# Performance work log

Measured on AMD Instinct MI355X. Metric: run time of the kernel, lower is better.

Reference implementation:

```python
import jax, jax.numpy as jnp
import numpy as np

HEAD_SIZE = 64
N_EMBED = 768
B, T = 16, 2048


def setup_inputs() -> dict:
    key = jax.random.key(0)
    ks = jax.random.split(key, 7)
    return {
        "x": jax.random.normal(ks[0], (B, T, N_EMBED), dtype=jnp.float32),
        "v1": jax.random.normal(ks[1], (B, T, HEAD_SIZE), dtype=jnp.float32),
        "Wk": jax.random.normal(ks[2], (N_EMBED, HEAD_SIZE), dtype=jnp.float32) * 0.02,
        "Wq": jax.random.normal(ks[3], (N_EMBED, HEAD_SIZE), dtype=jnp.float32) * 0.02,
        "Wv": jax.random.normal(ks[4], (N_EMBED, HEAD_SIZE), dtype=jnp.float32) * 0.02,
        "Wproj": jax.random.normal(ks[5], (HEAD_SIZE, HEAD_SIZE), dtype=jnp.float32) * 0.02,
        "bproj": jnp.zeros((HEAD_SIZE,), dtype=jnp.float32),
        "lamb": jnp.float32(0.5),
    }


def reference(x, v1, Wk, Wq, Wv, Wproj, bproj, lamb):
    # x: [B, T, C]; single-head causal attention with value-residual mixing.
    k = x @ Wk  # [B, T, H]
    q = x @ Wq
    v = x @ Wv
    v = (1.0 - lamb) * v + lamb * v1  # value-residual mix
    scale = jnp.float32(1.0 / np.sqrt(HEAD_SIZE))
    w = jnp.einsum("bth,bsh->bts", q, k) * scale  # [B, T, T]
    t = x.shape[1]
    causal = jnp.tril(jnp.ones((t, t), dtype=bool))  # [T, T]
    w = jnp.where(causal, w, jnp.float32(-jnp.inf))
    w = jax.nn.softmax(w, axis=-1)
    # dropout is identity in eval mode
    out = jnp.einsum("bts,bsh->bth", w, v)  # [B, T, H]
    return out @ Wproj + bproj, v1
```

## Files before the change

kernel.cpp:

```cpp
#include <hip/hip_runtime.h>
#include <hip/hip_bf16.h>


constexpr int BATCH = 16;
constexpr int TSEQ  = 2048;
constexpr int CEMB  = 768;
constexpr int HS    = 64;
constexpr size_t NTOK    = (size_t)BATCH * TSEQ;
constexpr size_t OUTHALF = NTOK * HS;

typedef __bf16 bf16x4 __attribute__((ext_vector_type(4)));
typedef __bf16 bf16x8 __attribute__((ext_vector_type(8)));
typedef float  f32x4  __attribute__((ext_vector_type(4)));
typedef float  f32x16 __attribute__((ext_vector_type(16)));
typedef int    i32x4  __attribute__((ext_vector_type(4)));

__global__ __launch_bounds__(256) void prep_kernel(
    const float* __restrict__ wk, const float* __restrict__ wq,
    const float* __restrict__ wv, const float* __restrict__ wproj,
    __bf16* __restrict__ wt, __bf16* __restrict__ wpt)
{
    __shared__ __bf16 t[64][66];
    const int bid = blockIdx.x;
    if (bid < 36) {
        const int m = bid / 12, c0 = (bid % 12) * 64;
        const float* src = (m == 0) ? wk : (m == 1) ? wq : wv;
        for (int i = threadIdx.x; i < 4096; i += 256) {
            const int c = i >> 6, h = i & 63;
            t[c][h] = (__bf16)src[(size_t)(c0 + c) * HS + h];
        }
        __syncthreads();
        for (int i = threadIdx.x; i < 4096; i += 256) {
            const int h = i >> 6, c = i & 63;
            wt[(size_t)m * HS * CEMB + (size_t)h * CEMB + c0 + c] = t[c][h];
        }
    } else {
        for (int i = threadIdx.x; i < 4096; i += 256) {
            const int h = i >> 6, hp = i & 63;
            t[h][hp] = (__bf16)wproj[i];
        }
        __syncthreads();
        for (int i = threadIdx.x; i < 4096; i += 256) {
            const int hp = i >> 6, h = i & 63;
            wpt[i] = t[h][hp];
        }
    }
}

__global__ __launch_bounds__(256, 2) void qkv_kernel(
    const float* __restrict__ x,
    const float* __restrict__ v1,
    const __bf16* __restrict__ wt,
    const float* __restrict__ lamb_p,
    __bf16* __restrict__ kk,
    __bf16* __restrict__ qq,
    __bf16* __restrict__ vt,
    float* __restrict__ v1out)
{
    __shared__ __bf16 xl[2][64][88];

    const int wave = threadIdx.x >> 6;
    const int lane = threadIdx.x & 63;
    const int l16  = lane & 15;
    const int quad = lane >> 4;
    const size_t row0 = (size_t)blockIdx.x * 64;

    const int tok_s = threadIdx.x >> 2;
    const int cq    = threadIdx.x & 3;
    const float* xsrc = x + (row0 + tok_s) * CEMB + cq * 16;

    const __bf16* wbase[3];
    #pragma unroll
    for (int m = 0; m < 3; ++m)
        wbase[m] = wt + ((size_t)m * HS + wave * 16 + l16) * CEMB + quad * 8;

    f32x4 acc[3][4];
    #pragma unroll
    for (int m = 0; m < 3; ++m)
        #pragma unroll
        for (int rt = 0; rt < 4; ++rt)
            acc[m][rt] = (f32x4){0.f, 0.f, 0.f, 0.f};

    {
        f32x4 t0 = *(const f32x4*)(xsrc);
        f32x4 t1 = *(const f32x4*)(xsrc + 4);
        f32x4 t2 = *(const f32x4*)(xsrc + 8);
        f32x4 t3 = *(const f32x4*)(xsrc + 12);
        bf16x8 lo, hi;
        #pragma unroll
        for (int i = 0; i < 4; ++i) {
            lo[i] = (__bf16)t0[i]; lo[i + 4] = (__bf16)t1[i];
            hi[i] = (__bf16)t2[i]; hi[i + 4] = (__bf16)t3[i];
        }
        *(bf16x8*)&xl[0][tok_s][cq * 16]     = lo;
        *(bf16x8*)&xl[0][tok_s][cq * 16 + 8] = hi;
    }
    bf16x8 wc[3][2];
    #pragma unroll
    for (int m = 0; m < 3; ++m)
        #pragma unroll
        for (int ks = 0; ks < 2; ++ks)
            wc[m][ks] = *(const bf16x8*)(wbase[m] + ks * 32);
    __syncthreads();

    for (int c0 = 0; c0 < CEMB; c0 += 64) {
        const int buf = (c0 >> 6) & 1;
        const bool notlast = (c0 + 64 < CEMB);

        f32x4 nx0, nx1, nx2, nx3;
        bf16x8 wn[3][2];
        if (notlast) {
            const float* xs = xsrc + c0 + 64;
            nx0 = *(const f32x4*)(xs);
            nx1 = *(const f32x4*)(xs + 4);
            nx2 = *(const f32x4*)(xs + 8);
            nx3 = *(const f32x4*)(xs + 12);
            #pragma unroll
            for (int m = 0; m < 3; ++m)
                #pragma unroll
                for (int ks = 0; ks < 2; ++ks)
                    wn[m][ks] = *(const bf16x8*)(wbase[m] + c0 + 64 + ks * 32);
        }

        #pragma unroll
        for (int ks = 0; ks < 2; ++ks) {
            bf16x8 a[4];
            #pragma unroll
            for (int rt = 0; rt < 4; ++rt)
                a[rt] = *(const bf16x8*)&xl[buf][rt * 16 + l16][ks * 32 + quad * 8];
            #pragma unroll
            for (int m = 0; m < 3; ++m)
                #pragma unroll
                for (int rt = 0; rt < 4; ++rt)
                    acc[m][rt] = __builtin_amdgcn_mfma_f32_16x16x32_bf16(
                        a[rt], wc[m][ks], acc[m][rt], 0, 0, 0);
        }

        if (notlast) {
            bf16x8 lo, hi;
            #pragma unroll
            for (int i = 0; i < 4; ++i) {
                lo[i] = (__bf16)nx0[i]; lo[i + 4] = (__bf16)nx1[i];
                hi[i] = (__bf16)nx2[i]; hi[i + 4] = (__bf16)nx3[i];
            }
            *(bf16x8*)&xl[buf ^ 1][tok_s][cq * 16]     = lo;
            *(bf16x8*)&xl[buf ^ 1][tok_s][cq * 16 + 8] = hi;
            #pragma unroll
            for (int m = 0; m < 3; ++m)
                #pragma unroll
                for (int ks = 0; ks < 2; ++ks)
                    wc[m][ks] = wn[m][ks];
            __syncthreads();
        }
    }

    const float lam = lamb_p[0];
    const int col = wave * 16 + l16;
    const int b  = (int)(row0 >> 11);
    __bf16* vtb = vt + (size_t)b * HS * TSEQ + (size_t)col * TSEQ;
    #pragma unroll
    for (int rt = 0; rt < 4; ++rt) {
        const size_t tok0 = row0 + rt * 16 + quad * 4;
        bf16x4 pk;
        #pragma unroll
        for (int r = 0; r < 4; ++r) {
            const size_t idx = (tok0 + r) * HS + col;
            const float v1v = v1[idx];
            kk[idx] = (__bf16)acc[0][rt][r];
            qq[idx] = (__bf16)acc[1][rt][r];
            pk[r] = (__bf16)((1.0f - lam) * acc[2][rt][r] + lam * v1v);
            if (v1out) v1out[idx] = v1v;
        }
        *(bf16x4*)(vtb + (tok0 & 2047)) = pk;
    }
}

__device__ __forceinline__ int pk2(float lo, float hi) {
    unsigned short a = __builtin_bit_cast(unsigned short, (__bf16)lo);
    unsigned short b = __builtin_bit_cast(unsigned short, (__bf16)hi);
    return (int)((((unsigned)b) << 16) | (unsigned)a);
}
__device__ __forceinline__ bf16x8 make_bfrag(const float* p, int hi) {
    const int a0 = pk2(p[0], p[1]), a1 = pk2(p[2], p[3]);
    const int b0 = pk2(p[4], p[5]), b1 = pk2(p[6], p[7]);
    const int pa0 = __shfl_xor(a0, 32), pa1 = __shfl_xor(a1, 32);
    const int pb0 = __shfl_xor(b0, 32), pb1 = __shfl_xor(b1, 32);
    i32x4 w;
    w[0] = hi ? pb0 : a0;
    w[1] = hi ? pb1 : a1;
    w[2] = hi ? b0  : pa0;
    w[3] = hi ? b1  : pa1;
    return __builtin_bit_cast(bf16x8, w);
}

__global__ __launch_bounds__(256, 2) void attn_kernel(
    const __bf16* __restrict__ q,
    const __bf16* __restrict__ k,
    const __bf16* __restrict__ vt,
    const __bf16* __restrict__ wpt,
    const float* __restrict__ bproj,
    float* __restrict__ y)
{
    __shared__ float olds[4][64][32];
    __shared__ float mred[4][32];
    __shared__ float lred[4][32];

    const int b    = blockIdx.x >> 5;
    const int jp   = blockIdx.x & 31;
    const int wave = threadIdx.x >> 6;
    const int lane = threadIdx.x & 63;
    const int l31  = lane & 31;
    const int hi   = lane >> 5;
    const int hi8  = hi * 8;

    const __bf16* kb = k  + (size_t)b * TSEQ * HS;
    const __bf16* vb = vt + (size_t)b * HS * TSEQ;
    const float sc2 = 0.125f * 1.44269504f;

    bf16x8 wf[4];
    if (wave < 2) {
        const __bf16* wp = wpt + (size_t)(wave * 32 + l31) * HS + hi8;
        #pragma unroll
        for (int c = 0; c < 4; ++c) wf[c] = *(const bf16x8*)(wp + c * 16);
    }

    for (int pass = 0; pass < 2; ++pass) {
        const int j = pass ? (63 - jp) : jp;
        const size_t tok0 = (size_t)b * TSEQ + (size_t)j * 32;

        const __bf16* qp = q + (tok0 + l31) * HS + hi8;
        bf16x8 qf[4];
        #pragma unroll
        for (int c = 0; c < 4; ++c) qf[c] = *(const bf16x8*)(qp + c * 16);

        f32x16 o0, o1;
        #pragma unroll
        for (int r = 0; r < 16; ++r) { o0[r] = 0.f; o1[r] = 0.f; }
        float m_i = -1e30f, l_i = 0.f;

        bf16x8 kf[4], kn[4], vf[4], vn[4];
        if (wave <= j) {
            const int s0 = wave * 32;
            const __bf16* kp = kb + (size_t)(s0 + l31) * HS + hi8;
            #pragma unroll
            for (int c = 0; c < 4; ++c) kf[c] = *(const bf16x8*)(kp + c * 16);
            #pragma unroll
            for (int ht = 0; ht < 2; ++ht)
                #pragma unroll
                for (int c2 = 0; c2 < 2; ++c2)
                    vf[ht * 2 + c2] = *(const bf16x8*)(vb
                        + (size_t)(ht * 32 + l31) * TSEQ + s0 + c2 * 16 + hi8);
        }

        for (int t = wave; t <= j; t += 4) {
            const int s0 = t * 32;
            const bool more = (t + 4 <= j);
            if (more) {
                const int sn = s0 + 128;
                const __bf16* kp = kb + (size_t)(sn + l31) * HS + hi8;
                #pragma unroll
                for (int c = 0; c < 4; ++c) kn[c] = *(const bf16x8*)(kp + c * 16);
                #pragma unroll
                for (int ht = 0; ht < 2; ++ht)
                    #pragma unroll
                    for (int c2 = 0; c2 < 2; ++c2)
                        vn[ht * 2 + c2] = *(const bf16x8*)(vb
                            + (size_t)(ht * 32 + l31) * TSEQ + sn + c2 * 16 + hi8);
            }

            f32x16 s;
            #pragma unroll
            for (int r = 0; r < 16; ++r) s[r] = 0.f;
            __builtin_amdgcn_s_setprio(1);
            #pragma unroll
            for (int c = 0; c < 4; ++c)
                s = __builtin_amdgcn_mfma_f32_32x32x16_bf16(kf[c], qf[c], s, 0, 0, 0);
            __builtin_amdgcn_s_setprio(0);

            float p[16];
            if (t == j) {
                #pragma unroll
                for (int r = 0; r < 16; ++r) {
                    const int krow = (r & 3) + 8 * (r >> 2) + 4 * hi;
                    p[r] = (krow <= l31) ? s[r] * sc2 : -1e30f;
                }
            } else {
                #pragma unroll
                for (int r = 0; r < 16; ++r) p[r] = s[r] * sc2;
            }

            float x0 = fmaxf(p[0], p[1]),   x1 = fmaxf(p[2], p[3]);
            float x2 = fmaxf(p[4], p[5]),   x3 = fmaxf(p[6], p[7]);
            float x4 = fmaxf(p[8], p[9]),   x5 = fmaxf(p[10], p[11]);
            float x6 = fmaxf(p[12], p[13]), x7 = fmaxf(p[14], p[15]);
            float mx = fmaxf(fmaxf(fmaxf(x0, x1), fmaxf(x2, x3)),
                             fmaxf(fmaxf(x4, x5), fmaxf(x6, x7)));
            mx = fmaxf(mx, __shfl_xor(mx, 32));

            if (!__all(mx <= m_i + 8.f)) {
                const float mn = fmaxf(m_i, mx);
                const float alpha = exp2f(m_i - mn);
                m_i = mn;
                l_i *= alpha;
                #pragma unroll
                for (int r = 0; r < 16; ++r) { o0[r] *= alpha; o1[r] *= alpha; }
            }

            #pragma unroll
            for (int r = 0; r < 16; ++r) p[r] = exp2f(p[r] - m_i);

            float r0 = (p[0] + p[1]) + (p[2] + p[3]);
            float r1 = (p[4] + p[5]) + (p[6] + p[7]);
            float r2 = (p[8] + p[9]) + (p[10] + p[11]);
            float r3 = (p[12] + p[13]) + (p[14] + p[15]);
            float rs = (r0 + r1) + (r2 + r3);
            rs += __shfl_xor(rs, 32);
            l_i += rs;

            const bf16x8 fb0 = make_bfrag(&p[0], hi);
            const bf16x8 fb1 = make_bfrag(&p[8], hi);

            __builtin_amdgcn_s_setprio(1);
            o0 = __builtin_amdgcn_mfma_f32_32x32x16_bf16(vf[0], fb0, o0, 0, 0, 0);
            o0 = __builtin_amdgcn_mfma_f32_32x32x16_bf16(vf[1], fb1, o0, 0, 0, 0);
            o1 = __builtin_amdgcn_mfma_f32_32x32x16_bf16(vf[2], fb0, o1, 0, 0, 0);
            o1 = __builtin_amdgcn_mfma_f32_32x32x16_bf16(vf[3], fb1, o1, 0, 0, 0);
            __builtin_amdgcn_s_setprio(0);

            if (more) {
                #pragma unroll
                for (int c = 0; c < 4; ++c) { kf[c] = kn[c]; vf[c] = vn[c]; }
            }
        }

        #pragma unroll
        for (int r = 0; r < 16; ++r) {
            const int row = (r & 3) + 8 * (r >> 2) + 4 * hi;
            olds[wave][row][l31]      = o0[r];
            olds[wave][row + 32][l31] = o1[r];
        }
        if (lane < 32) { mred[wave][lane] = m_i; lred[wave][lane] = l_i; }
        __syncthreads();

        if (wave < 2) {
            float mw[4], lw[4];
            #pragma unroll
            for (int w = 0; w < 4; ++w) { mw[w] = mred[w][l31]; lw[w] = lred[w][l31]; }
            const float mg = fmaxf(fmaxf(mw[0], mw[1]), fmaxf(mw[2], mw[3]));
            float g[4], lg = 0.f;
            #pragma unroll
            for (int w = 0; w < 4; ++w) { g[w] = exp2f(mw[w] - mg); lg += g[w] * lw[w]; }
            const float inv = 1.0f / lg;

            float on[32];
            #pragma unroll
            for (int r = 0; r < 16; ++r) {
                const int row = (r & 3) + 8 * (r >> 2) + 4 * hi;
                float a0 = 0.f, a1 = 0.f;
                #pragma unroll
                for (int w = 0; w < 4; ++w) {
                    a0 += g[w] * olds[w][row][l31];
                    a1 += g[w] * olds[w][row + 32][l31];
                }
                on[r]      = a0 * inv;
                on[r + 16] = a1 * inv;
            }

            f32x16 res;
            #pragma unroll
            for (int r = 0; r < 16; ++r) res[r] = 0.f;
            #pragma unroll
            for (int c = 0; c < 4; ++c) {
                const bf16x8 ob = make_bfrag(&on[c * 8], hi);
                res = __builtin_amdgcn_mfma_f32_32x32x16_bf16(wf[c], ob, res, 0, 0, 0);
            }

            float* yp = y + (tok0 + l31) * HS + wave * 32;
            #pragma unroll
            for (int grp = 0; grp < 4; ++grp) {
                const f32x4 bb = *(const f32x4*)(bproj + wave * 32 + grp * 8 + 4 * hi);
                f32x4 o4;
                #pragma unroll
                for (int rr = 0; rr < 4; ++rr) o4[rr] = res[grp * 4 + rr] + bb[rr];
                *(f32x4*)(yp + grp * 8 + 4 * hi) = o4;
            }
        }
        __syncthreads();
    }
}

__global__ __launch_bounds__(256) void copy_kernel(
    const float* __restrict__ src, float* __restrict__ dst)
{
    const size_t i = ((size_t)blockIdx.x * 256 + threadIdx.x) * 4;
    *(f32x4*)(dst + i) = *(const f32x4*)(src + i);
}

extern "C" void kernel_launch(void* const* d_in, const int* in_sizes, int n_in,
                              void* d_out, int out_size, void* d_ws, size_t ws_size,
                              hipStream_t stream) {
    const float* x     = (const float*)d_in[0];
    const float* v1    = (const float*)d_in[1];
    const float* wk    = (const float*)d_in[2];
    const float* wq    = (const float*)d_in[3];
    const float* wv    = (const float*)d_in[4];
    const float* wproj = (const float*)d_in[5];
    const float* bproj = (const float*)d_in[6];
    const float* lamb  = (const float*)d_in[7];

    float* out = (float*)d_out;

    __bf16* qp  = (__bf16*)d_ws;
    __bf16* wt  = qp + OUTHALF;
    __bf16* wpt = wt + (size_t)3 * HS * CEMB;
    const size_t base_elems = OUTHALF + (size_t)3 * HS * CEMB + (size_t)HS * HS;
    const size_t need_bytes = (base_elems + 2 * OUTHALF) * sizeof(__bf16);

    __bf16* kp;
    __bf16* vtp;
    float*  v1out;
    const bool fused_v1 = (ws_size >= need_bytes);
    if (fused_v1) {
        kp    = wpt + (size_t)HS * HS;
        vtp   = kp + OUTHALF;
        v1out = out + OUTHALF;
    } else {
        kp    = (__bf16*)(out + OUTHALF);
        vtp   = kp + OUTHALF;
        v1out = nullptr;
    }

    prep_kernel<<<dim3(37), dim3(256), 0, stream>>>(wk, wq, wv, wproj, wt, wpt);

    qkv_kernel<<<dim3((int)(NTOK / 64)), dim3(256), 0, stream>>>(
        x, v1, wt, lamb, kp, qp, vtp, v1out);

    attn_kernel<<<dim3(BATCH * 32), dim3(256), 0, stream>>>(
        qp, kp, vtp, wpt, bproj, out);

    if (!fused_v1) {
        copy_kernel<<<dim3((int)(OUTHALF / (256 * 4))), dim3(256), 0, stream>>>(
            v1, out + OUTHALF);
    }
}
```

Before: 237.5 us.

## Halve block work in QKV and attention kernels, raise occupancy to four blocks

```diff
diff --git a/kernel.cpp b/kernel.cpp
--- a/kernel.cpp
+++ b/kernel.cpp
@@ -47,7 +47,7 @@
     }
 }
 
-__global__ __launch_bounds__(256, 2) void qkv_kernel(
+__global__ __launch_bounds__(256, 4) void qkv_kernel(
     const float* __restrict__ x,
     const float* __restrict__ v1,
     const __bf16* __restrict__ wt,
@@ -57,43 +57,37 @@
     __bf16* __restrict__ vt,
     float* __restrict__ v1out)
 {
-    __shared__ __bf16 xl[2][64][88];
+    __shared__ __bf16 xl[2][32][88];
 
     const int wave = threadIdx.x >> 6;
     const int lane = threadIdx.x & 63;
     const int l16  = lane & 15;
     const int quad = lane >> 4;
-    const size_t row0 = (size_t)blockIdx.x * 64;
-
-    const int tok_s = threadIdx.x >> 2;
-    const int cq    = threadIdx.x & 3;
-    const float* xsrc = x + (row0 + tok_s) * CEMB + cq * 16;
+    const size_t row0 = (size_t)blockIdx.x * 32;
+
+    const int tok_s = threadIdx.x >> 3;
+    const int cq    = threadIdx.x & 7;
+    const float* xsrc = x + (row0 + tok_s) * CEMB + cq * 8;
 
     const __bf16* wbase[3];
     #pragma unroll
     for (int m = 0; m < 3; ++m)
         wbase[m] = wt + ((size_t)m * HS + wave * 16 + l16) * CEMB + quad * 8;
 
-    f32x4 acc[3][4];
+    f32x4 acc[3][2];
     #pragma unroll
     for (int m = 0; m < 3; ++m)
         #pragma unroll
-        for (int rt = 0; rt < 4; ++rt)
+        for (int rt = 0; rt < 2; ++rt)
             acc[m][rt] = (f32x4){0.f, 0.f, 0.f, 0.f};
 
     {
         f32x4 t0 = *(const f32x4*)(xsrc);
         f32x4 t1 = *(const f32x4*)(xsrc + 4);
-        f32x4 t2 = *(const f32x4*)(xsrc + 8);
-        f32x4 t3 = *(const f32x4*)(xsrc + 12);
-        bf16x8 lo, hi;
-        #pragma unroll
-        for (int i = 0; i < 4; ++i) {
-            lo[i] = (__bf16)t0[i]; lo[i + 4] = (__bf16)t1[i];
-            hi[i] = (__bf16)t2[i]; hi[i + 4] = (__bf16)t3[i];
-        }
-        *(bf16x8*)&xl[0][tok_s][cq * 16]     = lo;
-        *(bf16x8*)&xl[0][tok_s][cq * 16 + 8] = hi;
+        bf16x8 v;
+        #pragma unroll
+        for (int i = 0; i < 4; ++i) { v[i] = (__bf16)t0[i]; v[i + 4] = (__bf16)t1[i]; }
+        *(bf16x8*)&xl[0][tok_s][cq * 8] = v;
     }
     bf16x8 wc[3][2];
     #pragma unroll
@@ -107,14 +101,12 @@
         const int buf = (c0 >> 6) & 1;
         const bool notlast = (c0 + 64 < CEMB);
 
-        f32x4 nx0, nx1, nx2, nx3;
+        f32x4 nx0, nx1;
         bf16x8 wn[3][2];
         if (notlast) {
             const float* xs = xsrc + c0 + 64;
             nx0 = *(const f32x4*)(xs);
             nx1 = *(const f32x4*)(xs + 4);
-            nx2 = *(const f32x4*)(xs + 8);
-            nx3 = *(const f32x4*)(xs + 12);
             #pragma unroll
             for (int m = 0; m < 3; ++m)
                 #pragma unroll
@@ -124,27 +116,23 @@
 
         #pragma unroll
         for (int ks = 0; ks < 2; ++ks) {
-            bf16x8 a[4];
-            #pragma unroll
-            for (int rt = 0; rt < 4; ++rt)
+            bf16x8 a[2];
+            #pragma unroll
+            for (int rt = 0; rt < 2; ++rt)
                 a[rt] = *(const bf16x8*)&xl[buf][rt * 16 + l16][ks * 32 + quad * 8];
             #pragma unroll
             for (int m = 0; m < 3; ++m)
                 #pragma unroll
-                for (int rt = 0; rt < 4; ++rt)
+                for (int rt = 0; rt < 2; ++rt)
                     acc[m][rt] = __builtin_amdgcn_mfma_f32_16x16x32_bf16(
                         a[rt], wc[m][ks], acc[m][rt], 0, 0, 0);
         }
 
         if (notlast) {
-            bf16x8 lo, hi;
-            #pragma unroll
-            for (int i = 0; i < 4; ++i) {
-                lo[i] = (__bf16)nx0[i]; lo[i + 4] = (__bf16)nx1[i];
-                hi[i] = (__bf16)nx2[i]; hi[i + 4] = (__bf16)nx3[i];
-            }
-            *(bf16x8*)&xl[buf ^ 1][tok_s][cq * 16]     = lo;
-            *(bf16x8*)&xl[buf ^ 1][tok_s][cq * 16 + 8] = hi;
+            bf16x8 v;
+            #pragma unroll
+            for (int i = 0; i < 4; ++i) { v[i] = (__bf16)nx0[i]; v[i + 4] = (__bf16)nx1[i]; }
+            *(bf16x8*)&xl[buf ^ 1][tok_s][cq * 8] = v;
             #pragma unroll
             for (int m = 0; m < 3; ++m)
                 #pragma unroll
@@ -159,7 +147,7 @@
     const int b  = (int)(row0 >> 11);
     __bf16* vtb = vt + (size_t)b * HS * TSEQ + (size_t)col * TSEQ;
     #pragma unroll
-    for (int rt = 0; rt < 4; ++rt) {
+    for (int rt = 0; rt < 2; ++rt) {
         const size_t tok0 = row0 + rt * 16 + quad * 4;
         bf16x4 pk;
         #pragma unroll
@@ -193,7 +181,7 @@
     return __builtin_bit_cast(bf16x8, w);
 }
 
-__global__ __launch_bounds__(256, 2) void attn_kernel(
+__global__ __launch_bounds__(256, 4) void attn_kernel(
     const __bf16* __restrict__ q,
     const __bf16* __restrict__ k,
     const __bf16* __restrict__ vt,
@@ -205,8 +193,8 @@
     __shared__ float mred[4][32];
     __shared__ float lred[4][32];
 
-    const int b    = blockIdx.x >> 5;
-    const int jp   = blockIdx.x & 31;
+    const int b    = blockIdx.x >> 6;
+    const int j    = blockIdx.x & 63;
     const int wave = threadIdx.x >> 6;
     const int lane = threadIdx.x & 63;
     const int l31  = lane & 31;
@@ -224,168 +212,164 @@
         for (int c = 0; c < 4; ++c) wf[c] = *(const bf16x8*)(wp + c * 16);
     }
 
-    for (int pass = 0; pass < 2; ++pass) {
-        const int j = pass ? (63 - jp) : jp;
-        const size_t tok0 = (size_t)b * TSEQ + (size_t)j * 32;
-
-        const __bf16* qp = q + (tok0 + l31) * HS + hi8;
-        bf16x8 qf[4];
-        #pragma unroll
-        for (int c = 0; c < 4; ++c) qf[c] = *(const bf16x8*)(qp + c * 16);
-
-        f32x16 o0, o1;
-        #pragma unroll
-        for (int r = 0; r < 16; ++r) { o0[r] = 0.f; o1[r] = 0.f; }
-        float m_i = -1e30f, l_i = 0.f;
-
-        bf16x8 kf[4], kn[4], vf[4], vn[4];
-        if (wave <= j) {
-            const int s0 = wave * 32;
-            const __bf16* kp = kb + (size_t)(s0 + l31) * HS + hi8;
-            #pragma unroll
-            for (int c = 0; c < 4; ++c) kf[c] = *(const bf16x8*)(kp + c * 16);
+    const size_t tok0 = (size_t)b * TSEQ + (size_t)j * 32;
+
+    const __bf16* qp = q + (tok0 + l31) * HS + hi8;
+    bf16x8 qf[4];
+    #pragma unroll
+    for (int c = 0; c < 4; ++c) qf[c] = *(const bf16x8*)(qp + c * 16);
+
+    f32x16 o0, o1;
+    #pragma unroll
+    for (int r = 0; r < 16; ++r) { o0[r] = 0.f; o1[r] = 0.f; }
+    float m_i = -1e30f, l_i = 0.f;
+
+    bf16x8 kf[4], kn[4], vf[4], vn[4];
+    if (wave <= j) {
+        const int s0 = wave * 32;
+        const __bf16* kp = kb + (size_t)(s0 + l31) * HS + hi8;
+        #pragma unroll
+        for (int c = 0; c < 4; ++c) kf[c] = *(const bf16x8*)(kp + c * 16);
+        #pragma unroll
+        for (int ht = 0; ht < 2; ++ht)
+            #pragma unroll
+            for (int c2 = 0; c2 < 2; ++c2)
+                vf[ht * 2 + c2] = *(const bf16x8*)(vb
+                    + (size_t)(ht * 32 + l31) * TSEQ + s0 + c2 * 16 + hi8);
+    }
+
+    for (int t = wave; t <= j; t += 4) {
+        const int s0 = t * 32;
+        const bool more = (t + 4 <= j);
+        if (more) {
+            const int sn = s0 + 128;
+            const __bf16* kp = kb + (size_t)(sn + l31) * HS + hi8;
+            #pragma unroll
+            for (int c = 0; c < 4; ++c) kn[c] = *(const bf16x8*)(kp + c * 16);
             #pragma unroll
             for (int ht = 0; ht < 2; ++ht)
                 #pragma unroll
                 for (int c2 = 0; c2 < 2; ++c2)
-                    vf[ht * 2 + c2] = *(const bf16x8*)(vb
-                        + (size_t)(ht * 32 + l31) * TSEQ + s0 + c2 * 16 + hi8);
-        }
-
-        for (int t = wave; t <= j; t += 4) {
-            const int s0 = t * 32;
-            const bool more = (t + 4 <= j);
-            if (more) {
-                const int sn = s0 + 128;
-                const __bf16* kp = kb + (size_t)(sn + l31) * HS + hi8;
-                #pragma unroll
-                for (int c = 0; c < 4; ++c) kn[c] = *(const bf16x8*)(kp + c * 16);
-                #pragma unroll
-                for (int ht = 0; ht < 2; ++ht)
-                    #pragma unroll
-                    for (int c2 = 0; c2 < 2; ++c2)
-                        vn[ht * 2 + c2] = *(const bf16x8*)(vb
-                            + (size_t)(ht * 32 + l31) * TSEQ + sn + c2 * 16 + hi8);
+                    vn[ht * 2 + c2] = *(const bf16x8*)(vb
+                        + (size_t)(ht * 32 + l31) * TSEQ + sn + c2 * 16 + hi8);
+        }
+
+        f32x16 s;
+        #pragma unroll
+        for (int r = 0; r < 16; ++r) s[r] = 0.f;
+        __builtin_amdgcn_s_setprio(1);
+        #pragma unroll
+        for (int c = 0; c < 4; ++c)
+            s = __builtin_amdgcn_mfma_f32_32x32x16_bf16(kf[c], qf[c], s, 0, 0, 0);
+        __builtin_amdgcn_s_setprio(0);
+
+        float p[16];
+        if (t == j) {
+            #pragma unroll
+            for (int r = 0; r < 16; ++r) {
+                const int krow = (r & 3) + 8 * (r >> 2) + 4 * hi;
+                p[r] = (krow <= l31) ? s[r] * sc2 : -1e30f;
             }
-
-            f32x16 s;
-            #pragma unroll
-            for (int r = 0; r < 16; ++r) s[r] = 0.f;
-            __builtin_amdgcn_s_setprio(1);
-            #pragma unroll
-            for (int c = 0; c < 4; ++c)
-                s = __builtin_amdgcn_mfma_f32_32x32x16_bf16(kf[c], qf[c], s, 0, 0, 0);
-            __builtin_amdgcn_s_setprio(0);
-
-            float p[16];
-            if (t == j) {
-                #pragma unroll
-                for (int r = 0; r < 16; ++r) {
-                    const int krow = (r & 3) + 8 * (r >> 2) + 4 * hi;
-                    p[r] = (krow <= l31) ? s[r] * sc2 : -1e30f;
-                }
-            } else {
-                #pragma unroll
-                for (int r = 0; r < 16; ++r) p[r] = s[r] * sc2;
-            }
-
-            float x0 = fmaxf(p[0], p[1]),   x1 = fmaxf(p[2], p[3]);
-            float x2 = fmaxf(p[4], p[5]),   x3 = fmaxf(p[6], p[7]);
-            float x4 = fmaxf(p[8], p[9]),   x5 = fmaxf(p[10], p[11]);
-            float x6 = fmaxf(p[12], p[13]), x7 = fmaxf(p[14], p[15]);
-            float mx = fmaxf(fmaxf(fmaxf(x0, x1), fmaxf(x2, x3)),
-                             fmaxf(fmaxf(x4, x5), fmaxf(x6, x7)));
-            mx = fmaxf(mx, __shfl_xor(mx, 32));
-
-            if (!__all(mx <= m_i + 8.f)) {
-                const float mn = fmaxf(m_i, mx);
-                const float alpha = exp2f(m_i - mn);
-                m_i = mn;
-                l_i *= alpha;
-                #pragma unroll
-                for (int r = 0; r < 16; ++r) { o0[r] *= alpha; o1[r] *= alpha; }
-            }
-
-            #pragma unroll
-            for (int r = 0; r < 16; ++r) p[r] = exp2f(p[r] - m_i);
-
-            float r0 = (p[0] + p[1]) + (p[2] + p[3]);
-            float r1 = (p[4] + p[5]) + (p[6] + p[7]);
-            float r2 = (p[8] + p[9]) + (p[10] + p[11]);
-            float r3 = (p[12] + p[13]) + (p[14] + p[15]);
-            float rs = (r0 + r1) + (r2 + r3);
-            rs += __shfl_xor(rs, 32);
-            l_i += rs;
-
-            const bf16x8 fb0 = make_bfrag(&p[0], hi);
-            const bf16x8 fb1 = make_bfrag(&p[8], hi);
-
-            __builtin_amdgcn_s_setprio(1);
-            o0 = __builtin_amdgcn_mfma_f32_32x32x16_bf16(vf[0], fb0, o0, 0, 0, 0);
-            o0 = __builtin_amdgcn_mfma_f32_32x32x16_bf16(vf[1], fb1, o0, 0, 0, 0);
-            o1 = __builtin_amdgcn_mfma_f32_32x32x16_bf16(vf[2], fb0, o1, 0, 0, 0);
-            o1 = __builtin_amdgcn_mfma_f32_32x32x16_bf16(vf[3], fb1, o1, 0, 0, 0);
-            __builtin_amdgcn_s_setprio(0);
-
-            if (more) {
-                #pragma unroll
-                for (int c = 0; c < 4; ++c) { kf[c] = kn[c]; vf[c] = vn[c]; }
-            }
-        }
-
+        } else {
+            #pragma unroll
+            for (int r = 0; r < 16; ++r) p[r] = s[r] * sc2;
+        }
+
+        float x0 = fmaxf(p[0], p[1]),   x1 = fmaxf(p[2], p[3]);
+        float x2 = fmaxf(p[4], p[5]),   x3 = fmaxf(p[6], p[7]);
+        float x4 = fmaxf(p[8], p[9]),   x5 = fmaxf(p[10], p[11]);
+        float x6 = fmaxf(p[12], p[13]), x7 = fmaxf(p[14], p[15]);
+        float mx = fmaxf(fmaxf(fmaxf(x0, x1), fmaxf(x2, x3)),
+                         fmaxf(fmaxf(x4, x5), fmaxf(x6, x7)));
+        mx = fmaxf(mx, __shfl_xor(mx, 32));
+
+        if (!__all(mx <= m_i + 8.f)) {
+            const float mn = fmaxf(m_i, mx);
+            const float alpha = exp2f(m_i - mn);
+            m_i = mn;
+            l_i *= alpha;
+            #pragma unroll
+            for (int r = 0; r < 16; ++r) { o0[r] *= alpha; o1[r] *= alpha; }
+        }
+
+        #pragma unroll
+        for (int r = 0; r < 16; ++r) p[r] = exp2f(p[r] - m_i);
+
+        float r0 = (p[0] + p[1]) + (p[2] + p[3]);
+        float r1 = (p[4] + p[5]) + (p[6] + p[7]);
+        float r2 = (p[8] + p[9]) + (p[10] + p[11]);
+        float r3 = (p[12] + p[13]) + (p[14] + p[15]);
+        float rs = (r0 + r1) + (r2 + r3);
+        rs += __shfl_xor(rs, 32);
+        l_i += rs;
+
+        const bf16x8 fb0 = make_bfrag(&p[0], hi);
+        const bf16x8 fb1 = make_bfrag(&p[8], hi);
+
+        __builtin_amdgcn_s_setprio(1);
+        o0 = __builtin_amdgcn_mfma_f32_32x32x16_bf16(vf[0], fb0, o0, 0, 0, 0);
+        o0 = __builtin_amdgcn_mfma_f32_32x32x16_bf16(vf[1], fb1, o0, 0, 0, 0);
+        o1 = __builtin_amdgcn_mfma_f32_32x32x16_bf16(vf[2], fb0, o1, 0, 0, 0);
+        o1 = __builtin_amdgcn_mfma_f32_32x32x16_bf16(vf[3], fb1, o1, 0, 0, 0);
+        __builtin_amdgcn_s_setprio(0);
+
+        if (more) {
+            #pragma unroll
+            for (int c = 0; c < 4; ++c) { kf[c] = kn[c]; vf[c] = vn[c]; }
+        }
+    }
+
+    #pragma unroll
+    for (int r = 0; r < 16; ++r) {
+        const int row = (r & 3) + 8 * (r >> 2) + 4 * hi;
+        olds[wave][row][l31]      = o0[r];
+        olds[wave][row + 32][l31] = o1[r];
+    }
+    if (lane < 32) { mred[wave][lane] = m_i; lred[wave][lane] = l_i; }
+    __syncthreads();
+
+    if (wave < 2) {
+        float mw[4], lw[4];
+        #pragma unroll
+        for (int w = 0; w < 4; ++w) { mw[w] = mred[w][l31]; lw[w] = lred[w][l31]; }
+        const float mg = fmaxf(fmaxf(mw[0], mw[1]), fmaxf(mw[2], mw[3]));
+        float g[4], lg = 0.f;
+        #pragma unroll
+        for (int w = 0; w < 4; ++w) { g[w] = exp2f(mw[w] - mg); lg += g[w] * lw[w]; }
+        const float inv = 1.0f / lg;
+
+        float on[32];
         #pragma unroll
         for (int r = 0; r < 16; ++r) {
             const int row = (r & 3) + 8 * (r >> 2) + 4 * hi;
-            olds[wave][row][l31]      = o0[r];
-            olds[wave][row + 32][l31] = o1[r];
-        }
-        if (lane < 32) { mred[wave][lane] = m_i; lred[wave][lane] = l_i; }
-        __syncthreads();
-
-        if (wave < 2) {
-            float mw[4], lw[4];
-            #pragma unroll
-            for (int w = 0; w < 4; ++w) { mw[w] = mred[w][l31]; lw[w] = lred[w][l31]; }
-            const float mg = fmaxf(fmaxf(mw[0], mw[1]), fmaxf(mw[2], mw[3]));
-            float g[4], lg = 0.f;
-            #pragma unroll
-            for (int w = 0; w < 4; ++w) { g[w] = exp2f(mw[w] - mg); lg += g[w] * lw[w]; }
-            const float inv = 1.0f / lg;
-
-            float on[32];
-            #pragma unroll
-            for (int r = 0; r < 16; ++r) {
-                const int row = (r & 3) + 8 * (r >> 2) + 4 * hi;
-                float a0 = 0.f, a1 = 0.f;
-                #pragma unroll
-                for (int w = 0; w < 4; ++w) {
-                    a0 += g[w] * olds[w][row][l31];
-                    a1 += g[w] * olds[w][row + 32][l31];
-                }
-                on[r]      = a0 * inv;
-                on[r + 16] = a1 * inv;
+            float a0 = 0.f, a1 = 0.f;
+            #pragma unroll
+            for (int w = 0; w < 4; ++w) {
+                a0 += g[w] * olds[w][row][l31];
+                a1 += g[w] * olds[w][row + 32][l31];
             }
-
-            f32x16 res;
-            #pragma unroll
-            for (int r = 0; r < 16; ++r) res[r] = 0.f;
-            #pragma unroll
-            for (int c = 0; c < 4; ++c) {
-                const bf16x8 ob = make_bfrag(&on[c * 8], hi);
-                res = __builtin_amdgcn_mfma_f32_32x32x16_bf16(wf[c], ob, res, 0, 0, 0);
-            }
-
-            float* yp = y + (tok0 + l31) * HS + wave * 32;
-            #pragma unroll
-            for (int grp = 0; grp < 4; ++grp) {
-                const f32x4 bb = *(const f32x4*)(bproj + wave * 32 + grp * 8 + 4 * hi);
-                f32x4 o4;
-                #pragma unroll
-                for (int rr = 0; rr < 4; ++rr) o4[rr] = res[grp * 4 + rr] + bb[rr];
-                *(f32x4*)(yp + grp * 8 + 4 * hi) = o4;
-            }
-        }
-        __syncthreads();
+            on[r]      = a0 * inv;
+            on[r + 16] = a1 * inv;
+        }
+
+        f32x16 res;
+        #pragma unroll
+        for (int r = 0; r < 16; ++r) res[r] = 0.f;
+        #pragma unroll
+        for (int c = 0; c < 4; ++c) {
+            const bf16x8 ob = make_bfrag(&on[c * 8], hi);
+            res = __builtin_amdgcn_mfma_f32_32x32x16_bf16(wf[c], ob, res, 0, 0, 0);
+        }
+
+        float* yp = y + (tok0 + l31) * HS + wave * 32;
+        #pragma unroll
+        for (int grp = 0; grp < 4; ++grp) {
+            const f32x4 bb = *(const f32x4*)(bproj + wave * 32 + grp * 8 + 4 * hi);
+            f32x4 o4;
+            #pragma unroll
+            for (int rr = 0; rr < 4; ++rr) o4[rr] = res[grp * 4 + rr] + bb[rr];
+            *(f32x4*)(yp + grp * 8 + 4 * hi) = o4;
+        }
     }
 }
 
@@ -432,10 +416,10 @@
 
     prep_kernel<<<dim3(37), dim3(256), 0, stream>>>(wk, wq, wv, wproj, wt, wpt);
 
-    qkv_kernel<<<dim3((int)(NTOK / 64)), dim3(256), 0, stream>>>(
+    qkv_kernel<<<dim3((int)(NTOK / 32)), dim3(256), 0, stream>>>(
         x, v1, wt, lamb, kp, qp, vtp, v1out);
 
-    attn_kernel<<<dim3(BATCH * 32), dim3(256), 0, stream>>>(
+    attn_kernel<<<dim3(BATCH * 64), dim3(256), 0, stream>>>(
         qp, kp, vtp, wpt, bproj, out);
 
     if (!fused_v1) {
```

Result: slower. 311.6 us (+31.2%).
